# Performance work log

Measured on AMD Instinct MI355X. Metric: run time of the kernel, lower is better.

## Reference

```python
import jax, jax.numpy as jnp
import numpy as np

N = 50000
E = 800000
D = 128
EPS = 1e-5


def setup_inputs() -> dict:
    key = jax.random.key(0)
    ks = jax.random.split(key, 12)
    x = jax.random.normal(ks[0], (N, D), dtype=jnp.float32)
    pos = jax.random.normal(ks[1], (N, 3), dtype=jnp.float32)
    edge_index = jax.random.randint(ks[2], (2, E), 0, N, dtype=jnp.int32)
    s_e1 = 1.0 / np.sqrt(2 * D + 1)
    s_d = 1.0 / np.sqrt(D)
    s_n1 = 1.0 / np.sqrt(2 * D)
    return {
        "x": x,
        "pos": pos,
        "edge_index": edge_index,
        "W1e": jax.random.uniform(ks[3], (2 * D + 1, D), jnp.float32, -s_e1, s_e1),
        "b1e": jnp.zeros((D,), jnp.float32),
        "W2e": jax.random.uniform(ks[4], (D, D), jnp.float32, -s_d, s_d),
        "b2e": jnp.zeros((D,), jnp.float32),
        "W1n": jax.random.uniform(ks[5], (2 * D, D), jnp.float32, -s_n1, s_n1),
        "b1n": jnp.zeros((D,), jnp.float32),
        "W2n": jax.random.uniform(ks[6], (D, D), jnp.float32, -s_d, s_d),
        "b2n": jnp.zeros((D,), jnp.float32),
        "gamma": jnp.ones((D,), jnp.float32),
        "beta": jnp.zeros((D,), jnp.float32),
    }


def reference(x, pos, edge_index, W1e, b1e, W2e, b2e, W1n, b1n, W2n, b2n, gamma, beta):
    row, col = edge_index[0], edge_index[1]
    # gather + relative position
    rel_pos = pos[row] - pos[col]                       # [E, 3]
    dist2 = jnp.sum(rel_pos * rel_pos, axis=1, keepdims=True)  # [E, 1]
    edge_input = jnp.concatenate([x[row], x[col], dist2], axis=1)  # [E, 2D+1]
    # 2-layer edge MLP with SiLU activations
    h = jax.nn.silu(edge_input @ W1e + b1e)
    edge_feat = jax.nn.silu(h @ W2e + b2e)              # [E, D]
    # scatter-add aggregation onto source nodes (row)
    agg = jax.ops.segment_sum(edge_feat, row, num_segments=x.shape[0])  # [N, D]
    # 2-layer node MLP (SiLU only after first layer)
    node_in = jnp.concatenate([x, agg], axis=1)         # [N, 2D]
    update = jax.nn.silu(node_in @ W1n + b1n) @ W2n + b2n
    # dropout omitted (inference/eval mode)
    # LayerNorm(x + update)
    y = x + update
    mu = jnp.mean(y, axis=-1, keepdims=True)
    var = jnp.var(y, axis=-1, keepdims=True)
    return (y - mu) * jax.lax.rsqrt(var + EPS) * gamma + beta
```

## Files before the change

kernel.cpp:

```cpp
#include <hip/hip_runtime.h>
#include <hip/hip_bf16.h>
#include <math.h>

#define D 128
#define NND 50000
#define NE 800000
#define NB1 196
#define TPITCH 152

typedef __attribute__((ext_vector_type(8))) short shortx8;
typedef __attribute__((ext_vector_type(4))) float floatx4;
typedef __attribute__((ext_vector_type(4))) unsigned int uintx4;

__device__ __forceinline__ float silu_f(float v) {
    return v * __builtin_amdgcn_rcpf(1.0f + __expf(-v));
}
__device__ __forceinline__ unsigned short f2bf(float f) {
    union { float f; unsigned int u; } v; v.f = f;
    unsigned int u = v.u;
    u += 0x7fffu + ((u >> 16) & 1u);
    return (unsigned short)(u >> 16);
}
__device__ __forceinline__ void unpk(unsigned int u, float& lo, float& hi) {
    union { unsigned int x; float f; } a, b;
    a.x = u << 16;
    b.x = u & 0xffff0000u;
    lo = a.f; hi = b.f;
}

__global__ void zero_kernel(float4* __restrict__ p, int n4) {
    int i = blockIdx.x * blockDim.x + threadIdx.x;
    float4 z = make_float4(0.f, 0.f, 0.f, 0.f);
    for (; i < n4; i += gridDim.x * blockDim.x) p[i] = z;
}

__global__ void hist_kernel(const int* __restrict__ ei, int* __restrict__ deg) {
    int e = blockIdx.x * 256 + threadIdx.x;
    atomicAdd(&deg[ei[e]], 1);
}

__global__ void scan1_kernel(const int* __restrict__ deg,
                             int* __restrict__ part, int* __restrict__ bsum) {
    __shared__ int s[256];
    const int tid = threadIdx.x;
    const int i = blockIdx.x * 256 + tid;
    int v = (i < NND) ? deg[i] : 0;
    s[tid] = v;
    __syncthreads();
    #pragma unroll
    for (int off = 1; off < 256; off <<= 1) {
        int t = (tid >= off) ? s[tid - off] : 0;
        __syncthreads();
        s[tid] += t;
        __syncthreads();
    }
    part[i] = s[tid] - v;
    if (tid == 255) bsum[blockIdx.x] = s[255];
}

__global__ void scan2_kernel(const int* __restrict__ bsum, int* __restrict__ boff) {
    __shared__ int s[256];
    const int tid = threadIdx.x;
    int v = (tid < NB1) ? bsum[tid] : 0;
    s[tid] = v;
    __syncthreads();
    #pragma unroll
    for (int off = 1; off < 256; off <<= 1) {
        int t = (tid >= off) ? s[tid - off] : 0;
        __syncthreads();
        s[tid] += t;
        __syncthreads();
    }
    if (tid < NB1) boff[tid] = s[tid] - v;
}

__global__ void scan3_kernel(const int* __restrict__ part, const int* __restrict__ boff,
                             int* __restrict__ rowptr, int* __restrict__ cursor) {
    int i = blockIdx.x * 256 + threadIdx.x;
    if (i < NND) {
        int v = part[i] + boff[i >> 8];
        rowptr[i] = v;
        cursor[i] = v;
    } else if (i == NND) {
        rowptr[NND] = NE;
    }
}

__global__ void scatter_kernel(const int* __restrict__ ei, const float* __restrict__ pos,
                               int* __restrict__ cursor,
                               uint4* __restrict__ epack) {
    int e = blockIdx.x * 256 + threadIdx.x;
    int r = ei[e], c = ei[NE + e];
    float dx = pos[r * 3 + 0] - pos[c * 3 + 0];
    float dy = pos[r * 3 + 1] - pos[c * 3 + 1];
    float dz = pos[r * 3 + 2] - pos[c * 3 + 2];
    float d2 = dx * dx + dy * dy + dz * dz;
    int slot = atomicAdd(&cursor[r], 1);
    uint4 v;
    v.x = (unsigned int)c;
    v.y = (unsigned int)r;
    v.z = __float_as_uint(d2);
    v.w = 0u;
    epack[slot] = v;
}

__global__ void wswzall_kernel(const float* __restrict__ W1e, const float* __restrict__ W1n,
                               const float* __restrict__ W2e, const float* __restrict__ W2n,
                               unsigned short* __restrict__ w1f, unsigned short* __restrict__ w1nf,
                               unsigned short* __restrict__ w2f, unsigned short* __restrict__ w2nf,
                               unsigned short* __restrict__ wlf) {
    const int b = blockIdx.x;
    const float* W; unsigned short* Wf; int lb;
    if (b < 128)      { W = W1e; Wf = w1f;  lb = b; }
    else if (b < 256) { W = W1n; Wf = w1nf; lb = b - 128; }
    else if (b < 320) { W = W2e; Wf = w2f;  lb = b - 256; }
    else if (b < 384) { W = W2n; Wf = w2nf; lb = b - 320; }
    else {
        if (threadIdx.x < 128) wlf[threadIdx.x] = f2bf(W1e[256 * D + threadIdx.x]);
        return;
    }
    int f = lb * 256 + threadIdx.x;
    int j    = f & 7;
    int mrow = (f >> 3) & 15;
    int n    = (f >> 7) & 7;
    int rest = f >> 10;
    int quad = rest & 3;
    int ks   = rest >> 2;
    int col = n * 16 + mrow;
    int k   = ks * 32 + quad * 8 + j;
    Wf[f] = f2bf(W[k * D + col]);
}

__global__ __launch_bounds__(256) void precompute_kernel(
        const float* __restrict__ x,
        const unsigned short* __restrict__ w1f,
        const float* __restrict__ b1e,
        unsigned short* __restrict__ A,
        unsigned short* __restrict__ Bm) {
    const int t    = threadIdx.x;
    const int wv   = t >> 6;
    const int lane = t & 63;
    const int mrow = lane & 15;
    const int quad = lane >> 4;
    const int tile = blockIdx.x * 4 + wv;
    if (tile >= 3125) return;
    const int n0 = tile * 16;

    const float4* xrow = (const float4*)(x + ((size_t)(n0 + mrow) << 7));
    const uint4* wp   = (const uint4*)w1f;

    floatx4 accA[8], accB[8];
    #pragma unroll
    for (int n = 0; n < 8; ++n) {
        accA[n] = (floatx4){0.f, 0.f, 0.f, 0.f};
        accB[n] = (floatx4){0.f, 0.f, 0.f, 0.f};
    }

    #pragma unroll
    for (int s = 0; s < 4; ++s) {
        float4 xa = xrow[(s * 4 + quad) * 2 + 0];
        float4 xb = xrow[(s * 4 + quad) * 2 + 1];
        union { shortx8 v; __hip_bfloat162 p[4]; } af;
        af.p[0] = __float22bfloat162_rn(float2{xa.x, xa.y});
        af.p[1] = __float22bfloat162_rn(float2{xa.z, xa.w});
        af.p[2] = __float22bfloat162_rn(float2{xb.x, xb.y});
        af.p[3] = __float22bfloat162_rn(float2{xb.z, xb.w});
        const int baseA = (s * 4 + quad) * 128 + mrow;
        const int baseB = ((s + 4) * 4 + quad) * 128 + mrow;
        #pragma unroll
        for (int n = 0; n < 8; ++n) {
            union { uint4 u; shortx8 v; } bfA, bfB;
            bfA.u = wp[baseA + n * 16];
            bfB.u = wp[baseB + n * 16];
            accA[n] = __builtin_amdgcn_mfma_f32_16x16x32_bf16(af.v, bfA.v, accA[n], 0, 0, 0);
            accB[n] = __builtin_amdgcn_mfma_f32_16x16x32_bf16(af.v, bfB.v, accB[n], 0, 0, 0);
        }
    }

    float bb[8];
    #pragma unroll
    for (int n = 0; n < 8; ++n) bb[n] = b1e[n * 16 + mrow];

    #pragma unroll
    for (int reg = 0; reg < 4; ++reg) {
        const int node = n0 + quad * 4 + reg;
        #pragma unroll
        for (int n = 0; n < 8; ++n) {
            const int col = n * 16 + mrow;
            A[(size_t)node * D + col]  = f2bf(accA[n][reg] + bb[n]);
            Bm[(size_t)node * D + col] = f2bf(accB[n][reg]);
        }
    }
}

__global__ __launch_bounds__(256, 2) void edgemlp_kernel(
        const unsigned short* __restrict__ Abf,
        const unsigned short* __restrict__ Bbf,
        const uint4* __restrict__ epack,
        const unsigned short* __restrict__ wlf,
        const unsigned short* __restrict__ W2f,
        const float* __restrict__ b2e,
        unsigned short* __restrict__ ef) {
    const int t    = threadIdx.x;
    const int wv   = t >> 6;
    const int lane = t & 63;
    const int mrow = lane & 15;
    const int quad = lane >> 4;
    const int tile = blockIdx.x * 4 + wv;
    const int e0   = tile * 16;
    const int eme  = e0 + mrow;

    const uint4 ep = epack[eme];
    const int   c  = (int)ep.x;
    const int   r  = (int)ep.y;
    const float d2 = __uint_as_float(ep.z);

    const uint4* arow = (const uint4*)(Abf + ((size_t)r << 7));
    const uint4* brow = (const uint4*)(Bbf + ((size_t)c << 7));
    const uint4* wlq  = (const uint4*)wlf;
    const uint4* w2p  = (const uint4*)W2f;

    uint4 au[4], bu[4], wu[4];
    #pragma unroll
    for (int s = 0; s < 4; ++s) {
        au[s] = arow[s * 4 + quad];
        bu[s] = brow[s * 4 + quad];
        wu[s] = wlq[s * 4 + quad];
    }

    floatx4 acc[8];
    #pragma unroll
    for (int k = 0; k < 8; ++k) acc[k] = (floatx4){0.f, 0.f, 0.f, 0.f};

    #pragma unroll
    for (int s = 0; s < 4; ++s) {
        float a0, a1, a2, a3, a4, a5, a6, a7;
        float q0, q1, q2, q3, q4, q5, q6, q7;
        float w0, w1, w2, w3, w4, w5, w6, w7;
        unpk(au[s].x, a0, a1); unpk(au[s].y, a2, a3);
        unpk(au[s].z, a4, a5); unpk(au[s].w, a6, a7);
        unpk(bu[s].x, q0, q1); unpk(bu[s].y, q2, q3);
        unpk(bu[s].z, q4, q5); unpk(bu[s].w, q6, q7);
        unpk(wu[s].x, w0, w1); unpk(wu[s].y, w2, w3);
        unpk(wu[s].z, w4, w5); unpk(wu[s].w, w6, w7);

        float h0 = silu_f(fmaf(d2, w0, a0 + q0));
        float h1 = silu_f(fmaf(d2, w1, a1 + q1));
        float h2 = silu_f(fmaf(d2, w2, a2 + q2));
        float h3 = silu_f(fmaf(d2, w3, a3 + q3));
        float h4 = silu_f(fmaf(d2, w4, a4 + q4));
        float h5 = silu_f(fmaf(d2, w5, a5 + q5));
        float h6 = silu_f(fmaf(d2, w6, a6 + q6));
        float h7 = silu_f(fmaf(d2, w7, a7 + q7));

        union { shortx8 v; __hip_bfloat162 p[4]; } af;
        af.p[0] = __float22bfloat162_rn(float2{h0, h1});
        af.p[1] = __float22bfloat162_rn(float2{h2, h3});
        af.p[2] = __float22bfloat162_rn(float2{h4, h5});
        af.p[3] = __float22bfloat162_rn(float2{h6, h7});

        const int base = (s * 4 + quad) * 128 + mrow;
        #pragma unroll
        for (int k = 0; k < 8; ++k) {
            union { uint4 u; shortx8 v; } bf;
            bf.u = w2p[base + k * 16];
            acc[k] = __builtin_amdgcn_mfma_f32_16x16x32_bf16(af.v, bf.v, acc[k], 0, 0, 0);
        }
    }

    float bias[8];
    #pragma unroll
    for (int k = 0; k < 8; ++k) bias[k] = b2e[k * 16 + mrow];

    #pragma unroll
    for (int reg = 0; reg < 4; ++reg) {
        const int edge = e0 + quad * 4 + reg;
        union { uint4 u; __hip_bfloat162 p[4]; } ov;
        #pragma unroll
        for (int n = 0; n < 4; ++n) {
            float v0 = silu_f(acc[2 * n + 0][reg] + bias[2 * n + 0]);
            float v1 = silu_f(acc[2 * n + 1][reg] + bias[2 * n + 1]);
            ov.p[n] = __float22bfloat162_rn(float2{v0, v1});
        }
        *(uint4*)(ef + (((size_t)edge) << 7) + mrow * 8) = ov.u;
    }
}

__global__ __launch_bounds__(256) void aggsum_kernel(
        const unsigned short* __restrict__ ef,
        const int* __restrict__ rowptr,
        float* __restrict__ aggf) {
    const int t    = threadIdx.x;
    const int lane = t & 63;
    const int node = blockIdx.x * 4 + (t >> 6);
    const int start = rowptr[node];
    const int end   = rowptr[node + 1];
    const int sub  = lane >> 4;
    const int j    = lane & 15;

    const uintx4* ef4 = (const uintx4*)ef;

    float s[8];
    #pragma unroll
    for (int i = 0; i < 8; ++i) s[i] = 0.f;

    for (int e = start; e < end; e += 4) {
        const int  er    = e + sub;
        const bool valid = er < end;
        const int  safe  = valid ? er : start;
        uintx4 u = __builtin_nontemporal_load(ef4 + (size_t)safe * 16 + j);
        float f0, f1, f2, f3, f4, f5, f6, f7;
        unpk(u.x, f0, f1); unpk(u.y, f2, f3);
        unpk(u.z, f4, f5); unpk(u.w, f6, f7);
        if (valid) {
            s[0] += f0; s[1] += f1; s[2] += f2; s[3] += f3;
            s[4] += f4; s[5] += f5; s[6] += f6; s[7] += f7;
        }
    }
    #pragma unroll
    for (int i = 0; i < 8; ++i) {
        s[i] += __shfl_xor(s[i], 16);
        s[i] += __shfl_xor(s[i], 32);
    }
    if (sub == 0) {
        float* dst = aggf + ((size_t)node << 7) + j;
        #pragma unroll
        for (int i = 0; i < 8; ++i) dst[i * 16] = s[i];
    }
}

__global__ __launch_bounds__(256, 2) void edgeagg_kernel(
        const unsigned short* __restrict__ Abf,
        const unsigned short* __restrict__ Bbf,
        const int* __restrict__ rowptr,
        const uint4* __restrict__ epack,
        const unsigned short* __restrict__ wlf,
        const unsigned short* __restrict__ W2f,
        const float* __restrict__ b2e,
        float* __restrict__ aggf) {
    const int t    = threadIdx.x;
    const int wv   = t >> 6;
    const int lane = t & 63;
    const int mrow = lane & 15;
    const int quad = lane >> 4;
    const int node = blockIdx.x * 4 + wv;

    const int start = rowptr[node];
    const int d     = rowptr[node + 1] - start;

    const uint4* arow = (const uint4*)(Abf + ((size_t)node << 7));
    const uint4* wlq  = (const uint4*)wlf;
    uint4 au[4], wlu[4];
    #pragma unroll
    for (int s = 0; s < 4; ++s) {
        au[s]  = arow[s * 4 + quad];
        wlu[s] = wlq[s * 4 + quad];
    }
    float bias[8];
    #pragma unroll
    for (int k = 0; k < 8; ++k) bias[k] = b2e[k * 16 + mrow];

    float nacc[8];
    #pragma unroll
    for (int k = 0; k < 8; ++k) nacc[k] = 0.f;

    const uint4* w2p = (const uint4*)W2f;

    for (int tb = 0; tb < d; tb += 16) {
        const int  ei16 = tb + mrow;
        const bool ve   = ei16 < d;
        const int  idx  = start + (ve ? ei16 : 0);
        const uint4 ep  = epack[idx];
        const int  c    = (int)ep.x;
        float d2        = __uint_as_float(ep.z);
        d2 = ve ? d2 : 0.f;
        const uint4* brow = (const uint4*)(Bbf + ((size_t)c << 7));

        floatx4 acc[8];
        #pragma unroll
        for (int k = 0; k < 8; ++k) acc[k] = (floatx4){0.f, 0.f, 0.f, 0.f};

        #pragma unroll
        for (int s = 0; s < 4; ++s) {
            uint4 bu = brow[s * 4 + quad];

            float a0, a1, a2, a3, a4, a5, a6, a7;
            float q0, q1, q2, q3, q4, q5, q6, q7;
            float w0, w1, w2, w3, w4, w5, w6, w7;
            unpk(au[s].x, a0, a1); unpk(au[s].y, a2, a3);
            unpk(au[s].z, a4, a5); unpk(au[s].w, a6, a7);
            unpk(bu.x, q0, q1); unpk(bu.y, q2, q3);
            unpk(bu.z, q4, q5); unpk(bu.w, q6, q7);
            unpk(wlu[s].x, w0, w1); unpk(wlu[s].y, w2, w3);
            unpk(wlu[s].z, w4, w5); unpk(wlu[s].w, w6, w7);

            float h0 = silu_f(fmaf(d2, w0, a0 + q0));
            float h1 = silu_f(fmaf(d2, w1, a1 + q1));
            float h2 = silu_f(fmaf(d2, w2, a2 + q2));
            float h3 = silu_f(fmaf(d2, w3, a3 + q3));
            float h4 = silu_f(fmaf(d2, w4, a4 + q4));
            float h5 = silu_f(fmaf(d2, w5, a5 + q5));
            float h6 = silu_f(fmaf(d2, w6, a6 + q6));
            float h7 = silu_f(fmaf(d2, w7, a7 + q7));

            union { shortx8 v; __hip_bfloat162 p[4]; } af;
            af.p[0] = __float22bfloat162_rn(float2{h0, h1});
            af.p[1] = __float22bfloat162_rn(float2{h2, h3});
            af.p[2] = __float22bfloat162_rn(float2{h4, h5});
            af.p[3] = __float22bfloat162_rn(float2{h6, h7});

            const int base = (s * 4 + quad) * 128 + mrow;
            #pragma unroll
            for (int k = 0; k < 8; ++k) {
                union { uint4 u; shortx8 v; } bf;
                bf.u = w2p[base + k * 16];
                acc[k] = __builtin_amdgcn_mfma_f32_16x16x32_bf16(af.v, bf.v, acc[k], 0, 0, 0);
            }
        }

        #pragma unroll
        for (int reg = 0; reg < 4; ++reg) {
            const bool vr = (tb + quad * 4 + reg) < d;
            #pragma unroll
            for (int k = 0; k < 8; ++k)
                nacc[k] += vr ? silu_f(acc[k][reg] + bias[k]) : 0.f;
        }
    }

    #pragma unroll
    for (int k = 0; k < 8; ++k) {
        float v = nacc[k];
        v += __shfl_xor(v, 16);
        v += __shfl_xor(v, 32);
        nacc[k] = v;
    }
    const int n8a = quad * 2, n8b = quad * 2 + 1;
    aggf[(size_t)node * D + n8a * 16 + mrow] = nacc[n8a];
    aggf[(size_t)node * D + n8b * 16 + mrow] = nacc[n8b];
}

__global__ __launch_bounds__(64) void node_kernel(
        const float* __restrict__ aggf,
        const unsigned short* __restrict__ w1nf,
        const float* __restrict__ b1n,
        const unsigned short* __restrict__ w2nf,
        const float* __restrict__ b2n,
        const float* __restrict__ x,
        const float* __restrict__ gamma,
        const float* __restrict__ beta,
        float* __restrict__ out) {
    __shared__ __align__(16) unsigned short ts[16 * TPITCH];
    const int lane = threadIdx.x;
    const int mrow = lane & 15;
    const int quad = lane >> 4;
    const int n0 = blockIdx.x * 16;

    const float4* xrow  = (const float4*)(x + ((size_t)(n0 + mrow) << 7));
    const float4* growf = (const float4*)(aggf + ((size_t)(n0 + mrow) << 7));
    const uint4*  w1p   = (const uint4*)w1nf;
    const uint4*  w2p   = (const uint4*)w2nf;

    floatx4 acc[8];
    #pragma unroll
    for (int n = 0; n < 8; ++n) {
        float b = b1n[n * 16 + mrow];
        acc[n] = (floatx4){b, b, b, b};
    }

    #pragma unroll
    for (int s = 0; s < 4; ++s) {
        float4 xa = xrow[(s * 4 + quad) * 2 + 0];
        float4 xb = xrow[(s * 4 + quad) * 2 + 1];
        union { shortx8 v; __hip_bfloat162 p[4]; } af;
        af.p[0] = __float22bfloat162_rn(float2{xa.x, xa.y});
        af.p[1] = __float22bfloat162_rn(float2{xa.z, xa.w});
        af.p[2] = __float22bfloat162_rn(float2{xb.x, xb.y});
        af.p[3] = __float22bfloat162_rn(float2{xb.z, xb.w});
        const int base = (s * 4 + quad) * 128 + mrow;
        #pragma unroll
        for (int n = 0; n < 8; ++n) {
            union { uint4 u; shortx8 v; } bf;
            bf.u = w1p[base + n * 16];
            acc[n] = __builtin_amdgcn_mfma_f32_16x16x32_bf16(af.v, bf.v, acc[n], 0, 0, 0);
        }
    }
    #pragma unroll
    for (int s = 0; s < 4; ++s) {
        float4 g0 = growf[(s * 4 + quad) * 2 + 0];
        float4 g1 = growf[(s * 4 + quad) * 2 + 1];
        union { shortx8 v; __hip_bfloat162 p[4]; } af;
        af.p[0] = __float22bfloat162_rn(float2{g0.x, g0.y});
        af.p[1] = __float22bfloat162_rn(float2{g0.z, g0.w});
        af.p[2] = __float22bfloat162_rn(float2{g1.x, g1.y});
        af.p[3] = __float22bfloat162_rn(float2{g1.z, g1.w});
        const int base = ((s + 4) * 4 + quad) * 128 + mrow;
        #pragma unroll
        for (int n = 0; n < 8; ++n) {
            union { uint4 u; shortx8 v; } bf;
            bf.u = w1p[base + n * 16];
            acc[n] = __builtin_amdgcn_mfma_f32_16x16x32_bf16(af.v, bf.v, acc[n], 0, 0, 0);
        }
    }

    #pragma unroll
    for (int reg = 0; reg < 4; ++reg) {
        const int m = quad * 4 + reg;
        #pragma unroll
        for (int n = 0; n < 8; ++n)
            ts[m * TPITCH + n * 16 + mrow] = f2bf(silu_f(acc[n][reg]));
    }
    __syncthreads();

    floatx4 acc2[8];
    #pragma unroll
    for (int n = 0; n < 8; ++n) {
        float b = b2n[n * 16 + mrow];
        acc2[n] = (floatx4){b, b, b, b};
    }
    #pragma unroll
    for (int s = 0; s < 4; ++s) {
        shortx8 af2 = *(const shortx8*)((const char*)ts +
                        mrow * (TPITCH * 2) + (s * 4 + quad) * 16);
        const int base = (s * 4 + quad) * 128 + mrow;
        #pragma unroll
        for (int n = 0; n < 8; ++n) {
            union { uint4 u; shortx8 v; } bf;
            bf.u = w2p[base + n * 16];
            acc2[n] = __builtin_amdgcn_mfma_f32_16x16x32_bf16(af2, bf.v, acc2[n], 0, 0, 0);
        }
    }

    float g[8], bt[8];
    #pragma unroll
    for (int n = 0; n < 8; ++n) {
        g[n]  = gamma[n * 16 + mrow];
        bt[n] = beta[n * 16 + mrow];
    }
    #pragma unroll
    for (int reg = 0; reg < 4; ++reg) {
        const int node = n0 + quad * 4 + reg;
        float u[8];
        float s1 = 0.f, s2 = 0.f;
        #pragma unroll
        for (int n = 0; n < 8; ++n) {
            u[n] = acc2[n][reg] + x[(size_t)node * D + n * 16 + mrow];
            s1 += u[n];
            s2 += u[n] * u[n];
        }
        #pragma unroll
        for (int off = 1; off < 16; off <<= 1) {
            s1 += __shfl_xor(s1, off);
            s2 += __shfl_xor(s2, off);
        }
        const float mu  = s1 * (1.f / 128.f);
        const float var = s2 * (1.f / 128.f) - mu * mu;
        const float rs  = rsqrtf(var + 1e-5f);
        #pragma unroll
        for (int n = 0; n < 8; ++n)
            out[(size_t)node * D + n * 16 + mrow] = (u[n] - mu) * rs * g[n] + bt[n];
    }
}

extern "C" void kernel_launch(void* const* d_in, const int* in_sizes, int n_in,
                              void* d_out, int out_size, void* d_ws, size_t ws_size,
                              hipStream_t stream) {
    const float* x     = (const float*)d_in[0];
    const float* pos   = (const float*)d_in[1];
    const int*   ei    = (const int*)d_in[2];
    const float* W1e   = (const float*)d_in[3];
    const float* b1e   = (const float*)d_in[4];
    const float* W2e   = (const float*)d_in[5];
    const float* b2e   = (const float*)d_in[6];
    const float* W1n   = (const float*)d_in[7];
    const float* b1n   = (const float*)d_in[8];
    const float* W2n   = (const float*)d_in[9];
    const float* b2n   = (const float*)d_in[10];
    const float* gamma = (const float*)d_in[11];
    const float* beta  = (const float*)d_in[12];
    float* out = (float*)d_out;

    int*            deg    = (int*)d_ws;
    int*            part   = deg + 50176;
    int*            bsum   = part + 50176;
    int*            boff   = bsum + 256;
    int*            rowptr = boff + 256;
    int*            cursor = rowptr + 50004;
    uint4*          epack  = (uint4*)(cursor + 50000);
    unsigned short* Abf    = (unsigned short*)(epack + NE);
    unsigned short* Bbf    = Abf + (size_t)NND * D;
    unsigned short* w1f    = Bbf + (size_t)NND * D;
    unsigned short* w1nf   = w1f + 256 * D;
    unsigned short* w2f    = w1nf + 256 * D;
    unsigned short* w2nf   = w2f + D * D;
    unsigned short* wlf    = w2nf + D * D;
    unsigned short* ef     = wlf + 128;

    const size_t need_big = (size_t)((char*)(ef + (size_t)NE * D) - (char*)d_ws);
    const bool bigws = ws_size >= need_big;

    float* aggf = bigws ? (float*)Abf : (float*)ef;

    zero_kernel<<<49, 256, 0, stream>>>((float4*)deg, 50176 / 4);

    hist_kernel<<<NE / 256, 256, 0, stream>>>(ei, deg);
    scan1_kernel<<<NB1, 256, 0, stream>>>(deg, part, bsum);
    scan2_kernel<<<1, 256, 0, stream>>>(bsum, boff);
    scan3_kernel<<<197, 256, 0, stream>>>(part, boff, rowptr, cursor);
    scatter_kernel<<<NE / 256, 256, 0, stream>>>(ei, pos, cursor, epack);

    wswzall_kernel<<<385, 256, 0, stream>>>(W1e, W1n, W2e, W2n,
                                            w1f, w1nf, w2f, w2nf, wlf);

    precompute_kernel<<<782, 256, 0, stream>>>(x, w1f, b1e, Abf, Bbf);

    if (bigws) {
        edgemlp_kernel<<<NE / 16 / 4, 256, 0, stream>>>(Abf, Bbf, epack,
                                                        wlf, w2f, b2e, ef);
        aggsum_kernel<<<NND / 4, 256, 0, stream>>>(ef, rowptr, aggf);
    } else {
        edgeagg_kernel<<<NND / 4, 256, 0, stream>>>(Abf, Bbf, rowptr, epack,
                                                    wlf, w2f, b2e, aggf);
    }

    node_kernel<<<NND / 16, 64, 0, stream>>>(aggf, w1nf, b1n, w2nf, b2n,
                                             x, gamma, beta, out);
}
```

Baseline: 396.4 us.

## Fuse edge MLP with segmented per-block reduction and head/tail combine

```diff
diff --git a/kernel.cpp b/kernel.cpp
--- a/kernel.cpp
+++ b/kernel.cpp
@@ -7,10 +7,10 @@
 #define NE 800000
 #define NB1 196
 #define TPITCH 152
+#define CPITCH 132
 
 typedef __attribute__((ext_vector_type(8))) short shortx8;
 typedef __attribute__((ext_vector_type(4))) float floatx4;
-typedef __attribute__((ext_vector_type(4))) unsigned int uintx4;
 
 __device__ __forceinline__ float silu_f(float v) {
     return v * __builtin_amdgcn_rcpf(1.0f + __expf(-v));
@@ -193,21 +193,25 @@
     }
 }
 
-__global__ __launch_bounds__(256, 2) void edgemlp_kernel(
+__global__ __launch_bounds__(256, 2) void edgered_kernel(
         const unsigned short* __restrict__ Abf,
         const unsigned short* __restrict__ Bbf,
         const uint4* __restrict__ epack,
         const unsigned short* __restrict__ wlf,
         const unsigned short* __restrict__ W2f,
         const float* __restrict__ b2e,
-        unsigned short* __restrict__ ef) {
+        float* __restrict__ hpart,
+        float* __restrict__ tpart,
+        float* __restrict__ aggf) {
+    __shared__ float cs[64][CPITCH];
+    __shared__ int   rn[64];
+
     const int t    = threadIdx.x;
     const int wv   = t >> 6;
     const int lane = t & 63;
     const int mrow = lane & 15;
     const int quad = lane >> 4;
-    const int tile = blockIdx.x * 4 + wv;
-    const int e0   = tile * 16;
+    const int e0   = blockIdx.x * 64 + wv * 16;
     const int eme  = e0 + mrow;
 
     const uint4 ep = epack[eme];
@@ -274,169 +278,61 @@
 
     #pragma unroll
     for (int reg = 0; reg < 4; ++reg) {
-        const int edge = e0 + quad * 4 + reg;
-        union { uint4 u; __hip_bfloat162 p[4]; } ov;
-        #pragma unroll
-        for (int n = 0; n < 4; ++n) {
-            float v0 = silu_f(acc[2 * n + 0][reg] + bias[2 * n + 0]);
-            float v1 = silu_f(acc[2 * n + 1][reg] + bias[2 * n + 1]);
-            ov.p[n] = __float22bfloat162_rn(float2{v0, v1});
-        }
-        *(uint4*)(ef + (((size_t)edge) << 7) + mrow * 8) = ov.u;
-    }
-}
-
-__global__ __launch_bounds__(256) void aggsum_kernel(
-        const unsigned short* __restrict__ ef,
+        const int row = wv * 16 + quad * 4 + reg;
+        #pragma unroll
+        for (int k = 0; k < 8; ++k)
+            cs[row][k * 16 + mrow] = silu_f(acc[k][reg] + bias[k]);
+    }
+    if (lane < 16) rn[wv * 16 + lane] = r;
+    __syncthreads();
+
+    if (wv < 2) {
+        const int col = wv * 64 + lane;
+        const size_t blk = blockIdx.x;
+        int i = 0;
+        while (i < 64) {
+            const int n = rn[i];
+            int j = i + 1;
+            while (j < 64 && rn[j] == n) ++j;
+            float s = 0.f;
+            for (int kk = i; kk < j; ++kk) s += cs[kk][col];
+            if (i == 0)        hpart[blk * 128 + col] = s;
+            else if (j == 64)  tpart[blk * 128 + col] = s;
+            else               aggf[(size_t)n * 128 + col] = s;
+            i = j;
+        }
+    }
+}
+
+__global__ __launch_bounds__(256) void combine_kernel(
+        const float* __restrict__ hpart,
+        const float* __restrict__ tpart,
         const int* __restrict__ rowptr,
         float* __restrict__ aggf) {
-    const int t    = threadIdx.x;
-    const int lane = t & 63;
-    const int node = blockIdx.x * 4 + (t >> 6);
+    const int lane = threadIdx.x & 63;
+    const int node = blockIdx.x * 4 + (threadIdx.x >> 6);
     const int start = rowptr[node];
     const int end   = rowptr[node + 1];
-    const int sub  = lane >> 4;
-    const int j    = lane & 15;
-
-    const uintx4* ef4 = (const uintx4*)ef;
-
-    float s[8];
-    #pragma unroll
-    for (int i = 0; i < 8; ++i) s[i] = 0.f;
-
-    for (int e = start; e < end; e += 4) {
-        const int  er    = e + sub;
-        const bool valid = er < end;
-        const int  safe  = valid ? er : start;
-        uintx4 u = __builtin_nontemporal_load(ef4 + (size_t)safe * 16 + j);
-        float f0, f1, f2, f3, f4, f5, f6, f7;
-        unpk(u.x, f0, f1); unpk(u.y, f2, f3);
-        unpk(u.z, f4, f5); unpk(u.w, f6, f7);
-        if (valid) {
-            s[0] += f0; s[1] += f1; s[2] += f2; s[3] += f3;
-            s[4] += f4; s[5] += f5; s[6] += f6; s[7] += f7;
-        }
-    }
-    #pragma unroll
-    for (int i = 0; i < 8; ++i) {
-        s[i] += __shfl_xor(s[i], 16);
-        s[i] += __shfl_xor(s[i], 32);
-    }
-    if (sub == 0) {
-        float* dst = aggf + ((size_t)node << 7) + j;
-        #pragma unroll
-        for (int i = 0; i < 8; ++i) dst[i * 16] = s[i];
-    }
-}
-
-__global__ __launch_bounds__(256, 2) void edgeagg_kernel(
-        const unsigned short* __restrict__ Abf,
-        const unsigned short* __restrict__ Bbf,
-        const int* __restrict__ rowptr,
-        const uint4* __restrict__ epack,
-        const unsigned short* __restrict__ wlf,
-        const unsigned short* __restrict__ W2f,
-        const float* __restrict__ b2e,
-        float* __restrict__ aggf) {
-    const int t    = threadIdx.x;
-    const int wv   = t >> 6;
-    const int lane = t & 63;
-    const int mrow = lane & 15;
-    const int quad = lane >> 4;
-    const int node = blockIdx.x * 4 + wv;
-
-    const int start = rowptr[node];
-    const int d     = rowptr[node + 1] - start;
-
-    const uint4* arow = (const uint4*)(Abf + ((size_t)node << 7));
-    const uint4* wlq  = (const uint4*)wlf;
-    uint4 au[4], wlu[4];
-    #pragma unroll
-    for (int s = 0; s < 4; ++s) {
-        au[s]  = arow[s * 4 + quad];
-        wlu[s] = wlq[s * 4 + quad];
-    }
-    float bias[8];
-    #pragma unroll
-    for (int k = 0; k < 8; ++k) bias[k] = b2e[k * 16 + mrow];
-
-    float nacc[8];
-    #pragma unroll
-    for (int k = 0; k < 8; ++k) nacc[k] = 0.f;
-
-    const uint4* w2p = (const uint4*)W2f;
-
-    for (int tb = 0; tb < d; tb += 16) {
-        const int  ei16 = tb + mrow;
-        const bool ve   = ei16 < d;
-        const int  idx  = start + (ve ? ei16 : 0);
-        const uint4 ep  = epack[idx];
-        const int  c    = (int)ep.x;
-        float d2        = __uint_as_float(ep.z);
-        d2 = ve ? d2 : 0.f;
-        const uint4* brow = (const uint4*)(Bbf + ((size_t)c << 7));
-
-        floatx4 acc[8];
-        #pragma unroll
-        for (int k = 0; k < 8; ++k) acc[k] = (floatx4){0.f, 0.f, 0.f, 0.f};
-
-        #pragma unroll
-        for (int s = 0; s < 4; ++s) {
-            uint4 bu = brow[s * 4 + quad];
-
-            float a0, a1, a2, a3, a4, a5, a6, a7;
-            float q0, q1, q2, q3, q4, q5, q6, q7;
-            float w0, w1, w2, w3, w4, w5, w6, w7;
-            unpk(au[s].x, a0, a1); unpk(au[s].y, a2, a3);
-            unpk(au[s].z, a4, a5); unpk(au[s].w, a6, a7);
-            unpk(bu.x, q0, q1); unpk(bu.y, q2, q3);
-            unpk(bu.z, q4, q5); unpk(bu.w, q6, q7);
-            unpk(wlu[s].x, w0, w1); unpk(wlu[s].y, w2, w3);
-            unpk(wlu[s].z, w4, w5); unpk(wlu[s].w, w6, w7);
-
-            float h0 = silu_f(fmaf(d2, w0, a0 + q0));
-            float h1 = silu_f(fmaf(d2, w1, a1 + q1));
-            float h2 = silu_f(fmaf(d2, w2, a2 + q2));
-            float h3 = silu_f(fmaf(d2, w3, a3 + q3));
-            float h4 = silu_f(fmaf(d2, w4, a4 + q4));
-            float h5 = silu_f(fmaf(d2, w5, a5 + q5));
-            float h6 = silu_f(fmaf(d2, w6, a6 + q6));
-            float h7 = silu_f(fmaf(d2, w7, a7 + q7));
-
-            union { shortx8 v; __hip_bfloat162 p[4]; } af;
-            af.p[0] = __float22bfloat162_rn(float2{h0, h1});
-            af.p[1] = __float22bfloat162_rn(float2{h2, h3});
-            af.p[2] = __float22bfloat162_rn(float2{h4, h5});
-            af.p[3] = __float22bfloat162_rn(float2{h6, h7});
-
-            const int base = (s * 4 + quad) * 128 + mrow;
-            #pragma unroll
-            for (int k = 0; k < 8; ++k) {
-                union { uint4 u; shortx8 v; } bf;
-                bf.u = w2p[base + k * 16];
-                acc[k] = __builtin_amdgcn_mfma_f32_16x16x32_bf16(af.v, bf.v, acc[k], 0, 0, 0);
-            }
-        }
-
-        #pragma unroll
-        for (int reg = 0; reg < 4; ++reg) {
-            const bool vr = (tb + quad * 4 + reg) < d;
-            #pragma unroll
-            for (int k = 0; k < 8; ++k)
-                nacc[k] += vr ? silu_f(acc[k][reg] + bias[k]) : 0.f;
-        }
-    }
-
-    #pragma unroll
-    for (int k = 0; k < 8; ++k) {
-        float v = nacc[k];
-        v += __shfl_xor(v, 16);
-        v += __shfl_xor(v, 32);
-        nacc[k] = v;
-    }
-    const int n8a = quad * 2, n8b = quad * 2 + 1;
-    aggf[(size_t)node * D + n8a * 16 + mrow] = nacc[n8a];
-    aggf[(size_t)node * D + n8b * 16 + mrow] = nacc[n8b];
+    float2* ag2 = (float2*)(aggf + ((size_t)node << 7));
+    const float2* h2 = (const float2*)hpart;
+    const float2* t2 = (const float2*)tpart;
+
+    if (start == end) { ag2[lane] = make_float2(0.f, 0.f); return; }
+    const int t0 = start >> 6, t1 = (end - 1) >> 6;
+    if (t0 == t1) {
+        if ((start & 63) == 0)    ag2[lane] = h2[(size_t)t0 * 64 + lane];
+        else if ((end & 63) == 0) ag2[lane] = t2[(size_t)t0 * 64 + lane];
+        return;
+    }
+    float2 a = ((start & 63) == 0) ? h2[(size_t)t0 * 64 + lane]
+                                   : t2[(size_t)t0 * 64 + lane];
+    for (int tt = t0 + 1; tt < t1; ++tt) {
+        float2 b = h2[(size_t)tt * 64 + lane];
+        a.x += b.x; a.y += b.y;
+    }
+    float2 b = h2[(size_t)t1 * 64 + lane];
+    a.x += b.x; a.y += b.y;
+    ag2[lane] = a;
 }
 
 __global__ __launch_bounds__(64) void node_kernel(
@@ -593,12 +489,9 @@
     unsigned short* w2f    = w1nf + 256 * D;
     unsigned short* w2nf   = w2f + D * D;
     unsigned short* wlf    = w2nf + D * D;
-    unsigned short* ef     = wlf + 128;
-
-    const size_t need_big = (size_t)((char*)(ef + (size_t)NE * D) - (char*)d_ws);
-    const bool bigws = ws_size >= need_big;
-
-    float* aggf = bigws ? (float*)Abf : (float*)ef;
+    float*          aggf   = (float*)(wlf + 128);
+    float*          hpart  = aggf + (size_t)NND * D;
+    float*          tpart  = hpart + (size_t)(NE / 64) * D;
 
     zero_kernel<<<49, 256, 0, stream>>>((float4*)deg, 50176 / 4);
 
@@ -613,14 +506,9 @@
 
     precompute_kernel<<<782, 256, 0, stream>>>(x, w1f, b1e, Abf, Bbf);
 
-    if (bigws) {
-        edgemlp_kernel<<<NE / 16 / 4, 256, 0, stream>>>(Abf, Bbf, epack,
-                                                        wlf, w2f, b2e, ef);
-        aggsum_kernel<<<NND / 4, 256, 0, stream>>>(ef, rowptr, aggf);
-    } else {
-        edgeagg_kernel<<<NND / 4, 256, 0, stream>>>(Abf, Bbf, rowptr, epack,
-                                                    wlf, w2f, b2e, aggf);
-    }
+    edgered_kernel<<<NE / 64, 256, 0, stream>>>(Abf, Bbf, epack, wlf, w2f, b2e,
+                                                hpart, tpart, aggf);
+    combine_kernel<<<NND / 4, 256, 0, stream>>>(hpart, tpart, rowptr, aggf);
 
     node_kernel<<<NND / 16, 64, 0, stream>>>(aggf, w1nf, b1n, w2nf, b2n,
                                              x, gamma, beta, out);
```

Measured after the change: 397.3 us. About the same (+0.2%).
